# Kernel optimization log

Hardware: AMD Instinct MI355X
Metric: run time of the kernel (lower is better)

Reference implementation:

```python
import jax, jax.numpy as jnp
import numpy as np

NU, NI, DU, DI, L, FD, G, B = 100000, 50000, 128, 128, 128, 64, 3, 16384
EU, EG = 1600000, 800000


def _seg_softmax(scores, seg, n):
    # numerically stable softmax over edges grouped by destination node
    m = jax.ops.segment_max(scores, seg, num_segments=n)
    e = jnp.exp(scores - m[seg])
    s = jax.ops.segment_sum(e, seg, num_segments=n)
    return e / s[seg]


def _gat(S, W1, a_s, a_n, src, dst, n, edge_w=None):
    H1 = S @ W1                                   # [n, L]
    sc = (H1 @ a_s)[dst] + (H1 @ a_n)[src]        # [E] alpha_self_i + alpha_nb_j
    if edge_w is not None:
        sc = edge_w * sc                          # omega weighting (multi-graph)
    sc = jax.nn.leaky_relu(sc, negative_slope=0.2)
    alpha = _seg_softmax(sc, dst, n)
    return jax.ops.segment_sum(H1[src] * alpha[:, None], dst, num_segments=n)


def setup_inputs() -> dict:
    rng = np.random.default_rng(0)
    eu = rng.integers(0, NU, size=(2, EU))
    # multi-graph item edges -> coalesce (dedup, per-graph counts) as torch_geometric.coalesce reduce='add'
    e_all = rng.integers(0, NI, size=(G, 2, EG))
    src = e_all[:, 0, :].reshape(-1)
    dst = e_all[:, 1, :].reshape(-1)
    codes = dst.astype(np.int64) * NI + src
    uniq, inv = np.unique(codes, return_inverse=True)
    counts = np.zeros((uniq.size, G), np.float32)
    gid = np.repeat(np.arange(G), EG)
    np.add.at(counts, (inv, gid), 1.0)
    eb = np.stack([uniq % NI, uniq // NI]).astype(np.int64)

    key = jax.random.key(0)
    ks = jax.random.split(key, 24)
    def nrm(k, shape, s):
        return (jax.random.normal(k, shape) * s).astype(jnp.float32)
    sL = 1.0 / np.sqrt(L)
    sD = 1.0 / np.sqrt(DU)
    return {
        'user_indices': jnp.asarray(rng.integers(0, NU, B), jnp.int32),
        'item_indices': jnp.asarray(rng.integers(0, NI, B), jnp.int32),
        'S_u': nrm(ks[0], (NU, DU), 1.0),
        'S_b': nrm(ks[1], (NI, DI), 1.0),
        'edge_index_u': jnp.asarray(eu, jnp.int32),
        'edge_index_b': jnp.asarray(eb, jnp.int32),
        'graph_counts': jnp.asarray(counts),
        'W1_u': nrm(ks[2], (DU, L), sD), 'a_self_u': nrm(ks[3], (L,), sL), 'a_nb_u': nrm(ks[4], (L,), sL),
        'W1_b': nrm(ks[5], (DI, L), sD), 'a_self_b': nrm(ks[6], (L,), sL), 'a_nb_b': nrm(ks[7], (L,), sL),
        'omega': jnp.full((G,), 1.0 / G, jnp.float32),
        'W_u2': nrm(ks[8], (L, L), sL), 'W_us2_w': nrm(ks[9], (DU, L), sD), 'W_us2_b': jnp.zeros((L,), jnp.float32),
        'W_b2': nrm(ks[10], (L, L), sL), 'W_bs2_w': nrm(ks[11], (DI, L), sD), 'W_bs2_b': jnp.zeros((L,), jnp.float32),
        'W_u3': nrm(ks[12], (L, FD), sL), 'W_b3': nrm(ks[13], (L, FD), sL),
        'H_u4': nrm(ks[14], (NU, FD), 0.01), 'H_b4': nrm(ks[15], (NI, FD), 0.01),
        'bias_u': jnp.zeros((NU,), jnp.float32), 'bias_b': jnp.zeros((NI,), jnp.float32),
        'b_x': jnp.zeros((), jnp.float32),
    }


def reference(user_indices, item_indices, S_u, S_b, edge_index_u, edge_index_b, graph_counts,
              W1_u, a_self_u, a_nb_u, W1_b, a_self_b, a_nb_b, omega,
              W_u2, W_us2_w, W_us2_b, W_b2, W_bs2_w, W_bs2_b,
              W_u3, W_b3, H_u4, H_b4, bias_u, bias_b, b_x):
    Hu2 = _gat(S_u, W1_u, a_self_u, a_nb_u, edge_index_u[0], edge_index_u[1], S_u.shape[0])
    uw = graph_counts @ omega                     # coalesced omega weights per unified edge
    Hb2 = _gat(S_b, W1_b, a_self_b, a_nb_b, edge_index_b[0], edge_index_b[1], S_b.shape[0], edge_w=uw)
    Hu3 = jax.nn.elu(Hu2 @ W_u2 + S_u @ W_us2_w + W_us2_b)
    Hb3 = jax.nn.elu(Hb2 @ W_b2 + S_b @ W_bs2_w + W_bs2_b)
    U = jax.nn.elu(Hu3 @ W_u3) + H_u4
    Bm = jax.nn.elu(Hb3 @ W_b3) + H_b4
    dot = (U[user_indices] * Bm[item_indices]).sum(-1)
    raw = dot + bias_u[user_indices] + bias_b[item_indices] + b_x
    return 4.0 * jax.nn.sigmoid(raw) + 1.0        # (r_max-r_min)*sigmoid + r_min
```

## Files before the change

kernel.cpp:

```cpp
#include <hip/hip_runtime.h>
#include <hip/hip_bf16.h>

#define KD 128
#define NANF __int_as_float(0x7fc00000)

typedef __attribute__((ext_vector_type(8))) short bf16x8;
typedef __attribute__((ext_vector_type(4))) float f32x4;

__device__ __forceinline__ unsigned short f2b(float x) {
  unsigned u = __float_as_uint(x);
  return (unsigned short)((u + 0x7fffu + ((u >> 16) & 1u)) >> 16);
}
__device__ __forceinline__ int swz(int row, int kbyte) {
  return (row * 256 + kbyte) ^ ((row & 7) << 4);
}

__global__ __launch_bounds__(256) void wsplit6(
    const float* __restrict__ w0, const float* __restrict__ w1,
    const float* __restrict__ w2, const float* __restrict__ w3,
    const float* __restrict__ w4, const float* __restrict__ w5,
    unsigned short* __restrict__ oh)
{
  int m = blockIdx.x >> 6;
  int idx = (blockIdx.x & 63) * 256 + threadIdx.x;
  const float* ws;
  switch (m) { case 0: ws = w0; break; case 1: ws = w1; break; case 2: ws = w2; break;
               case 3: ws = w3; break; case 4: ws = w4; break; default: ws = w5; }
  int n = idx >> 7, k = idx & 127;
  oh[(long)m * 16384 + idx] = f2b(ws[k * 128 + n]);
}

__global__ __launch_bounds__(256) void segb_kernel(
    const int* __restrict__ dst, int E,
    int* __restrict__ sstart, int* __restrict__ send)
{
  int e = blockIdx.x * 256 + threadIdx.x;
  if (e >= E) return;
  int d = dst[e];
  if (e == 0 || dst[e - 1] != d) sstart[d] = e;
  if (e == E - 1 || dst[e + 1] != d) send[d] = e + 1;
}

__global__ __launch_bounds__(256, 3) void mfma1_dual(
    int split,
    const float* __restrict__ Aa, const unsigned short* __restrict__ Wta, int Ma,
    unsigned short* __restrict__ Ca,
    const float* __restrict__ a_sa, const float* __restrict__ a_na,
    float* __restrict__ as_oa, float* __restrict__ an_oa, const unsigned char* __restrict__ fla,
    const float* __restrict__ Ab, const unsigned short* __restrict__ Wtb, int Mb,
    unsigned short* __restrict__ Cb,
    const float* __restrict__ a_sb, const float* __restrict__ a_nb,
    float* __restrict__ as_ob, float* __restrict__ an_ob, const unsigned char* __restrict__ flb)
{
  const bool sB = (int)blockIdx.x >= split;
  const float* A = sB ? Ab : Aa;
  const unsigned short* Wt = sB ? Wtb : Wta;
  const int M = sB ? Mb : Ma;
  unsigned short* C = sB ? Cb : Ca;
  const float* a_s = sB ? a_sb : a_sa;  const float* a_n = sB ? a_nb : a_na;
  float* as_o = sB ? as_ob : as_oa;     float* an_o = sB ? an_ob : an_oa;
  const unsigned char* fl = sB ? flb : fla;
  const int bid = sB ? ((int)blockIdx.x - split) : (int)blockIdx.x;

  __shared__ unsigned short sW[16384];
  __shared__ unsigned short sA[8192];
  __shared__ float pp[4][64][2];

  const int t = threadIdx.x;
  const int w = t >> 6, l = t & 63;
  const int lr = l & 15, lk = l >> 4;
  const int row0 = bid * 64;
  char* sWc = reinterpret_cast<char*>(sW);
  char* sAc = reinterpret_cast<char*>(sA);

  #pragma unroll
  for (int q = 0; q < 8; ++q) {
    int p = t + 256 * q;
    int n = p >> 4, c16 = p & 15;
    bf16x8 v = *reinterpret_cast<const bf16x8*>(Wt + n * 128 + c16 * 8);
    *reinterpret_cast<bf16x8*>(sWc + swz(n, c16 * 16)) = v;
  }
  #pragma unroll
  for (int q = 0; q < 4; ++q) {
    int p = t + 256 * q;
    int r = p >> 4, c16 = p & 15;
    int gr = row0 + r;
    bf16x8 hv;
    if (gr < M) {
      const float4* ap = reinterpret_cast<const float4*>(A + (long)gr * KD + c16 * 8);
      float4 v0 = ap[0], v1 = ap[1];
      hv[0]=(short)f2b(v0.x); hv[1]=(short)f2b(v0.y); hv[2]=(short)f2b(v0.z); hv[3]=(short)f2b(v0.w);
      hv[4]=(short)f2b(v1.x); hv[5]=(short)f2b(v1.y); hv[6]=(short)f2b(v1.z); hv[7]=(short)f2b(v1.w);
    } else {
      #pragma unroll
      for (int j = 0; j < 8; ++j) hv[j] = 0;
    }
    *reinterpret_cast<bf16x8*>(sAc + swz(r, c16 * 16)) = hv;
  }
  __syncthreads();

  f32x4 acc[4][2];
  #pragma unroll
  for (int i = 0; i < 4; ++i)
    #pragma unroll
    for (int tt = 0; tt < 2; ++tt) acc[i][tt] = (f32x4){0.f, 0.f, 0.f, 0.f};

  #pragma unroll
  for (int kc = 0; kc < 4; ++kc) {
    const int kb = (kc * 32 + lk * 8) * 2;
    bf16x8 af[4];
    #pragma unroll
    for (int i = 0; i < 4; ++i)
      af[i] = *reinterpret_cast<const bf16x8*>(sAc + swz(i * 16 + lr, kb));
    #pragma unroll
    for (int tt = 0; tt < 2; ++tt) {
      int n = (w * 2 + tt) * 16 + lr;
      bf16x8 bfr = *reinterpret_cast<const bf16x8*>(sWc + swz(n, kb));
      #pragma unroll
      for (int i = 0; i < 4; ++i)
        acc[i][tt] = __builtin_amdgcn_mfma_f32_16x16x32_bf16(af[i], bfr, acc[i][tt], 0, 0, 0);
    }
  }

  float asv[2], anv[2];
  #pragma unroll
  for (int tt = 0; tt < 2; ++tt) {
    int col = (w * 2 + tt) * 16 + lr;
    asv[tt] = a_s[col]; anv[tt] = a_n[col];
  }
  #pragma unroll
  for (int i = 0; i < 4; ++i) {
    #pragma unroll
    for (int r = 0; r < 4; ++r) {
      float ds = acc[i][0][r] * asv[0] + acc[i][1][r] * asv[1];
      float dn = acc[i][0][r] * anv[0] + acc[i][1][r] * anv[1];
      #pragma unroll
      for (int o = 1; o < 16; o <<= 1) { ds += __shfl_xor(ds, o, 64); dn += __shfl_xor(dn, o, 64); }
      if (lr == 0) {
        int row = i * 16 + lk * 4 + r;
        pp[w][row][0] = ds; pp[w][row][1] = dn;
      }
    }
  }
  #pragma unroll
  for (int i = 0; i < 4; ++i) {
    #pragma unroll
    for (int r = 0; r < 4; ++r) {
      int gr = row0 + i * 16 + lk * 4 + r;
      if (gr >= M) continue;
      #pragma unroll
      for (int tt = 0; tt < 2; ++tt) {
        int col = (w * 2 + tt) * 16 + lr;
        C[(long)gr * 128 + col] = f2b(acc[i][tt][r]);
      }
    }
  }
  __syncthreads();
  if (t < 64) {
    int gr = row0 + t;
    if (gr < M) {
      float ds = pp[0][t][0] + pp[1][t][0] + pp[2][t][0] + pp[3][t][0];
      float dn = pp[0][t][1] + pp[1][t][1] + pp[2][t][1] + pp[3][t][1];
      as_o[gr] = fl[gr] ? ds : NANF;
      an_o[gr] = dn;
    }
  }
}

__global__ __launch_bounds__(256, 3) void mfma2_dual(
    int split,
    const float* __restrict__ A1a, const unsigned short* __restrict__ W1ta,
    const float* __restrict__ A2a, const unsigned short* __restrict__ W2ta,
    const float* __restrict__ biasa, const int* __restrict__ aidxa,
    const int* __restrict__ map1a, int Ma, float* __restrict__ Ca,
    const float* __restrict__ A1b, const unsigned short* __restrict__ W1tb,
    const float* __restrict__ A2b, const unsigned short* __restrict__ W2tb,
    const float* __restrict__ biasb, const int* __restrict__ aidxb,
    const int* __restrict__ map1b, int Mb, float* __restrict__ Cb)
{
  const bool sB = (int)blockIdx.x >= split;
  const float* A1 = sB ? A1b : A1a;  const unsigned short* W1t = sB ? W1tb : W1ta;
  const float* A2 = sB ? A2b : A2a;  const unsigned short* W2t = sB ? W2tb : W2ta;
  const float* bias = sB ? biasb : biasa;
  const int* aidx = sB ? aidxb : aidxa;  const int* map1 = sB ? map1b : map1a;
  const int M = sB ? Mb : Ma;  float* C = sB ? Cb : Ca;
  const int bid = sB ? ((int)blockIdx.x - split) : (int)blockIdx.x;

  __shared__ unsigned short sW[16384];
  __shared__ unsigned short sA[8192];

  const int t = threadIdx.x;
  const int w = t >> 6, l = t & 63;
  const int lr = l & 15, lk = l >> 4;
  const int row0 = bid * 64;
  char* sWc = reinterpret_cast<char*>(sW);
  char* sAc = reinterpret_cast<char*>(sA);

  f32x4 acc[4][2];
  #pragma unroll
  for (int i = 0; i < 4; ++i)
    #pragma unroll
    for (int tt = 0; tt < 2; ++tt) acc[i][tt] = (f32x4){0.f, 0.f, 0.f, 0.f};

  #pragma unroll
  for (int pass = 0; pass < 2; ++pass) {
    const float* Am = pass ? A2 : A1;
    const unsigned short* Wt = pass ? W2t : W1t;
    if (pass) __syncthreads();
    #pragma unroll
    for (int q = 0; q < 8; ++q) {
      int p = t + 256 * q;
      int n = p >> 4, c16 = p & 15;
      bf16x8 v = *reinterpret_cast<const bf16x8*>(Wt + n * 128 + c16 * 8);
      *reinterpret_cast<bf16x8*>(sWc + swz(n, c16 * 16)) = v;
    }
    #pragma unroll
    for (int q = 0; q < 4; ++q) {
      int p = t + 256 * q;
      int r = p >> 4, c16 = p & 15;
      int gr = row0 + r;
      bf16x8 hv;
      if (gr < M) {
        long grow = (long)aidx[gr];
        if (pass == 0) grow = map1[grow];
        const float4* ap = reinterpret_cast<const float4*>(Am + grow * KD + c16 * 8);
        float4 v0 = ap[0], v1 = ap[1];
        hv[0]=(short)f2b(v0.x); hv[1]=(short)f2b(v0.y); hv[2]=(short)f2b(v0.z); hv[3]=(short)f2b(v0.w);
        hv[4]=(short)f2b(v1.x); hv[5]=(short)f2b(v1.y); hv[6]=(short)f2b(v1.z); hv[7]=(short)f2b(v1.w);
      } else {
        #pragma unroll
        for (int j = 0; j < 8; ++j) hv[j] = 0;
      }
      *reinterpret_cast<bf16x8*>(sAc + swz(r, c16 * 16)) = hv;
    }
    __syncthreads();
    #pragma unroll
    for (int kc = 0; kc < 4; ++kc) {
      const int kb = (kc * 32 + lk * 8) * 2;
      bf16x8 af[4];
      #pragma unroll
      for (int i = 0; i < 4; ++i)
        af[i] = *reinterpret_cast<const bf16x8*>(sAc + swz(i * 16 + lr, kb));
      #pragma unroll
      for (int tt = 0; tt < 2; ++tt) {
        int n = (w * 2 + tt) * 16 + lr;
        bf16x8 bfr = *reinterpret_cast<const bf16x8*>(sWc + swz(n, kb));
        #pragma unroll
        for (int i = 0; i < 4; ++i)
          acc[i][tt] = __builtin_amdgcn_mfma_f32_16x16x32_bf16(af[i], bfr, acc[i][tt], 0, 0, 0);
      }
    }
  }
  float bv[2];
  #pragma unroll
  for (int tt = 0; tt < 2; ++tt) bv[tt] = bias[(w * 2 + tt) * 16 + lr];
  #pragma unroll
  for (int i = 0; i < 4; ++i) {
    #pragma unroll
    for (int r = 0; r < 4; ++r) {
      int gr = row0 + i * 16 + lk * 4 + r;
      if (gr >= M) continue;
      #pragma unroll
      for (int tt = 0; tt < 2; ++tt) {
        int col = (w * 2 + tt) * 16 + lr;
        float v = acc[i][tt][r] + bv[tt];
        v = (v > 0.f) ? v : (__expf(v) - 1.f);
        C[(long)gr * 128 + col] = v;
      }
    }
  }
}

template<int BM, int NC>
__global__ __launch_bounds__(256, 3) void gemm3_dual(
    int split,
    const float* __restrict__ A1a, const float* __restrict__ W1a,
    const float* __restrict__ Resa, const int* __restrict__ ridxa, int Ma,
    float* __restrict__ Ca,
    const float* __restrict__ A1b, const float* __restrict__ W1b,
    const float* __restrict__ Resb, const int* __restrict__ ridxb, int Mb,
    float* __restrict__ Cb)
{
  const bool sB = (int)blockIdx.x >= split;
  const float* A1 = sB ? A1b : A1a;  const float* W1 = sB ? W1b : W1a;
  const float* Res = sB ? Resb : Resa;
  const int* ridx = sB ? ridxb : ridxa;
  const int M = sB ? Mb : Ma;  float* C = sB ? Cb : Ca;
  const int bid = sB ? ((int)blockIdx.x - split) : (int)blockIdx.x;

  constexpr int RT = BM / 16;
  constexpr int CW = NC / 16;
  constexpr int KB = 64;
  constexpr int CPP = KD / KB;
  constexpr int F4PR = KB / 4;
  constexpr int NAF4 = BM * KB / 4 / 256;
  constexpr int NWF4 = KB * NC / 4 / 256;
  __shared__ float sA[BM][KB + 4];
  __shared__ float sW[KB][NC];
  const int t  = threadIdx.x;
  const int ty = t >> 4, tx = t & 15;
  const int row0 = bid * BM;

  float acc[RT][CW];
  #pragma unroll
  for (int i = 0; i < RT; ++i)
    #pragma unroll
    for (int j = 0; j < CW; ++j) acc[i][j] = 0.f;

  for (int cc = 0; cc < CPP; ++cc) {
    const int kc = cc;
    if (cc) __syncthreads();
    {
      const float4* Wp = reinterpret_cast<const float4*>(W1) + (long)kc * (KB * NC / 4);
      #pragma unroll
      for (int q = 0; q < NWF4; ++q)
        reinterpret_cast<float4*>(&sW[0][0])[t + 256 * q] = Wp[t + 256 * q];
    }
    #pragma unroll
    for (int q = 0; q < NAF4; ++q) {
      int p  = t + 256 * q;
      int r  = p / F4PR, c4 = p % F4PR;
      float4 v = make_float4(0.f, 0.f, 0.f, 0.f);
      int gr = row0 + r;
      if (gr < M) {
        v = reinterpret_cast<const float4*>(A1 + (long)gr * KD)[kc * F4PR + c4];
      }
      *reinterpret_cast<float4*>(&sA[r][c4 * 4]) = v;
    }
    __syncthreads();
    #pragma unroll 4
    for (int k4 = 0; k4 < KB; k4 += 4) {
      float4 a4[RT];
      #pragma unroll
      for (int i = 0; i < RT; ++i)
        a4[i] = *reinterpret_cast<const float4*>(&sA[ty + 16 * i][k4]);
      #pragma unroll
      for (int kk = 0; kk < 4; ++kk) {
        float wv[CW];
        #pragma unroll
        for (int h = 0; h < CW / 4; ++h) {
          float4 w4 = *reinterpret_cast<const float4*>(&sW[k4 + kk][tx * 4 + 64 * h]);
          wv[h*4+0] = w4.x; wv[h*4+1] = w4.y; wv[h*4+2] = w4.z; wv[h*4+3] = w4.w;
        }
        #pragma unroll
        for (int i = 0; i < RT; ++i) {
          float a = (kk == 0) ? a4[i].x : (kk == 1) ? a4[i].y : (kk == 2) ? a4[i].z : a4[i].w;
          #pragma unroll
          for (int j = 0; j < CW; ++j)
            acc[i][j] = fmaf(a, wv[j], acc[i][j]);
        }
      }
    }
  }
  #pragma unroll
  for (int i = 0; i < RT; ++i) {
    int gr = row0 + ty + 16 * i;
    if (gr >= M) continue;
    long rrow = (long)ridx[gr];
    #pragma unroll
    for (int h = 0; h < CW / 4; ++h) {
      int c = tx * 4 + 64 * h;
      float4 v = make_float4(acc[i][h*4+0], acc[i][h*4+1], acc[i][h*4+2], acc[i][h*4+3]);
      v.x = (v.x > 0.f) ? v.x : (__expf(v.x) - 1.f);
      v.y = (v.y > 0.f) ? v.y : (__expf(v.y) - 1.f);
      v.z = (v.z > 0.f) ? v.z : (__expf(v.z) - 1.f);
      v.w = (v.w > 0.f) ? v.w : (__expf(v.w) - 1.f);
      float4 rv = *reinterpret_cast<const float4*>(Res + rrow * NC + c);
      v.x += rv.x; v.y += rv.y; v.z += rv.z; v.w += rv.w;
      *reinterpret_cast<float4*>(C + (long)gr * NC + c) = v;
    }
  }
}

__global__ void flags_kernel(const int* __restrict__ ui, const int* __restrict__ ii, int B,
                             unsigned char* __restrict__ nfu, unsigned char* __restrict__ nfb,
                             unsigned* __restrict__ mku, unsigned* __restrict__ mkb)
{
  int i = blockIdx.x * blockDim.x + threadIdx.x;
  if (i < B) {
    int u = ui[i], v = ii[i];
    nfu[u] = 1; nfb[v] = 1;
    atomicOr(&mku[u >> 5], 1u << (u & 31));
    atomicOr(&mkb[v >> 5], 1u << (v & 31));
  }
}

__global__ __launch_bounds__(256) void edge_prep_dual(
    int split,
    const int* __restrict__ srcA, const int* __restrict__ dstA,
    const float* __restrict__ asA, const float* __restrict__ anA,
    const unsigned* __restrict__ mkA, const int* __restrict__ ssA,
    int* __restrict__ degA, int4* __restrict__ cmpA, int* __restrict__ bcA, int EA,
    const int* __restrict__ srcB, const int* __restrict__ dstB,
    const float* __restrict__ asB, const float* __restrict__ anB,
    const unsigned* __restrict__ mkB, const int* __restrict__ ssB,
    const float* __restrict__ gc, const float* __restrict__ omega,
    int* __restrict__ degB, int4* __restrict__ cmpB, int* __restrict__ bcB, int EB_)
{
  const bool sB = (int)blockIdx.x >= split;
  const int* src = sB ? srcB : srcA;  const int* dst = sB ? dstB : dstA;
  const float* as_ = sB ? asB : asA;  const float* an_ = sB ? anB : anA;
  const unsigned* mk = sB ? mkB : mkA;
  const int* ss = sB ? ssB : ssA;
  int* deg = sB ? degB : degA;  int4* cmp = sB ? cmpB : cmpA;
  int* blkcnt = sB ? bcB : bcA;
  const int E = sB ? EB_ : EA;
  const float* gcp = sB ? gc : nullptr;
  const int bid = sB ? ((int)blockIdx.x - split) : (int)blockIdx.x;

  __shared__ int lcnt;
  if (threadIdx.x == 0) lcnt = 0;
  __syncthreads();
  const int lane = threadIdx.x & 63;
  const long base = (long)bid * 4096;
  const int e0 = (int)base + threadIdx.x * 16;

  int d[16], s[16];
  bool act[16];
  const bool full = (e0 + 15 < E);
  if (full) {
    #pragma unroll
    for (int q = 0; q < 4; ++q) {
      int4 d4 = *reinterpret_cast<const int4*>(dst + e0 + q * 4);
      int4 s4 = *reinterpret_cast<const int4*>(src + e0 + q * 4);
      d[q*4+0]=d4.x; d[q*4+1]=d4.y; d[q*4+2]=d4.z; d[q*4+3]=d4.w;
      s[q*4+0]=s4.x; s[q*4+1]=s4.y; s[q*4+2]=s4.z; s[q*4+3]=s4.w;
    }
    #pragma unroll
    for (int j = 0; j < 16; ++j) act[j] = true;
  } else {
    #pragma unroll
    for (int j = 0; j < 16; ++j) {
      act[j] = (e0 + j < E);
      d[j] = act[j] ? dst[e0 + j] : 0;
      s[j] = act[j] ? src[e0 + j] : 0;
    }
  }
  unsigned mw[16];
  #pragma unroll
  for (int j = 0; j < 16; ++j) mw[j] = mk[d[j] >> 5];
  #pragma unroll
  for (int j = 0; j < 16; ++j) act[j] = act[j] && ((mw[j] >> (d[j] & 31)) & 1u);

  float uw[16];
  if (gcp) {
    float o0 = omega[0], o1 = omega[1], o2 = omega[2];
    if (full) {
      float g[48];
      const float4* gp = reinterpret_cast<const float4*>(gcp + (long)e0 * 3);
      #pragma unroll
      for (int q = 0; q < 12; ++q) *reinterpret_cast<float4*>(&g[q*4]) = gp[q];
      #pragma unroll
      for (int j = 0; j < 16; ++j) uw[j] = g[j*3+0]*o0 + g[j*3+1]*o1 + g[j*3+2]*o2;
    } else {
      #pragma unroll
      for (int j = 0; j < 16; ++j) {
        uw[j] = 0.f;
        if (act[j]) {
          long e = e0 + j;
          uw[j] = gcp[e*3+0]*o0 + gcp[e*3+1]*o1 + gcp[e*3+2]*o2;
        }
      }
    }
  }
  float vas[16], van[16];
  #pragma unroll
  for (int j = 0; j < 16; ++j) vas[j] = act[j] ? as_[d[j]] : 0.f;
  #pragma unroll
  for (int j = 0; j < 16; ++j) van[j] = act[j] ? an_[s[j]] : 0.f;
  int ssv[16];
  if (ss) {
    #pragma unroll
    for (int j = 0; j < 16; ++j) ssv[j] = act[j] ? ss[d[j]] : 0;
  }
  float sc[16];
  #pragma unroll
  for (int j = 0; j < 16; ++j) {
    float v = vas[j] + van[j];
    if (gcp) v *= uw[j];
    v = (v >= 0.f) ? v : 0.2f * v;
    sc[j] = __expf(v);
  }
  int tot = 0;
  #pragma unroll
  for (int j = 0; j < 16; ++j) tot += __popcll(__ballot(act[j]));
  int wb = 0;
  if (lane == 0) wb = atomicAdd(&lcnt, tot);
  wb = __shfl(wb, 0, 64);
  #pragma unroll
  for (int j = 0; j < 16; ++j) {
    unsigned long long m = __ballot(act[j]);
    if (act[j]) {
      int pref = __popcll(m & ((1ull << lane) - 1ull));
      int rel = ss ? (e0 + j - ssv[j]) : atomicAdd(&deg[d[j]], 1);
      cmp[base + wb + pref] = make_int4(s[j], d[j], rel, __float_as_int(sc[j]));
    }
    wb += __popcll(m);
  }
  __syncthreads();
  if (threadIdx.x == 0) blkcnt[bid] = lcnt;
}

__global__ __launch_bounds__(256) void offset_dual(
    int split,
    const unsigned char* __restrict__ flA, int* __restrict__ degA,
    int* __restrict__ offsA, int* __restrict__ dlA, int* __restrict__ g2cA,
    int* __restrict__ cntA, int NA,
    const unsigned char* __restrict__ flB, int* __restrict__ degB,
    const int* __restrict__ sstartB, const int* __restrict__ sendB,
    int* __restrict__ offsB, int* __restrict__ dlB, int* __restrict__ g2cB,
    int* __restrict__ cntB, int NB)
{
  const bool sB = (int)blockIdx.x >= split;
  const unsigned char* flag = sB ? flB : flA;
  int* deg = sB ? degB : degA;
  int* offs = sB ? offsB : offsA;  int* dlist = sB ? dlB : dlA;
  int* g2c = sB ? g2cB : g2cA;     int* cnt = sB ? cntB : cntA;
  const int N = sB ? NB : NA;
  const int bid = sB ? ((int)blockIdx.x - split) : (int)blockIdx.x;
  const int lane = threadIdx.x & 63;

  int idx[4], dg[4], exc[4], prf[4], nwq[4], tq[4];
  bool av[4];
  int wn = 0, wt = 0;
  #pragma unroll
  for (int q = 0; q < 4; ++q) {
    int i = bid * 1024 + q * 256 + (int)threadIdx.x;
    idx[q] = i;
    bool a = (i < N) && flag[i];
    int dgv = 0;
    if (a) {
      if (sB) { dgv = sendB[i] - sstartB[i]; deg[i] = dgv; }
      else dgv = deg[i];
    }
    av[q] = a; dg[q] = dgv;
    unsigned long long m = __ballot(a);
    nwq[q] = __popcll(m);
    prf[q] = __popcll(m & ((1ull << lane) - 1ull));
    int inc = dgv;
    #pragma unroll
    for (int o = 1; o < 64; o <<= 1) {
      int v = __shfl_up(inc, o, 64);
      if (lane >= o) inc += v;
    }
    tq[q] = __shfl(inc, 63, 64);
    exc[q] = inc - dgv;
    wn += nwq[q]; wt += tq[q];
  }
  int baseL = 0, baseE = 0;
  if (lane == 0) {
    baseL = wn ? atomicAdd(&cnt[1], wn) : 0;
    baseE = wt ? atomicAdd(&cnt[0], wt) : 0;
  }
  baseL = __shfl(baseL, 0, 64);
  baseE = __shfl(baseE, 0, 64);
  int runN = 0, runE = 0;
  #pragma unroll
  for (int q = 0; q < 4; ++q) {
    if (av[q]) {
      int i = idx[q];
      int l = baseL + runN + prf[q];
      g2c[i] = l;
      dlist[l] = i;
      if (dg[q] > 0) offs[i] = baseE + runE + exc[q];
    }
    runN += nwq[q]; runE += tq[q];
  }
}

__global__ __launch_bounds__(256) void place_dual(
    int split,
    const int4* __restrict__ cmpA, const int* __restrict__ bcA,
    const int* __restrict__ offsA, int2* __restrict__ elA,
    const int4* __restrict__ cmpB, const int* __restrict__ bcB,
    const int* __restrict__ offsB, int2* __restrict__ elB)
{
  const bool sB = (int)blockIdx.x >= split;
  const int4* cmp = sB ? cmpB : cmpA;
  const int* blkcnt = sB ? bcB : bcA;
  const int* offs = sB ? offsB : offsA;
  int2* eline = sB ? elB : elA;
  const int bid = sB ? ((int)blockIdx.x - split) : (int)blockIdx.x;

  int nb = blkcnt[bid];
  const long base = (long)bid * 4096;
  for (int k = threadIdx.x; k < nb; k += 256) {
    int4 c = cmp[base + k];
    int pos = offs[c.y] + c.z;
    eline[pos] = make_int2(c.x, c.w);
  }
}

__global__ __launch_bounds__(256) void aggr_dual(
    int split,
    const int* __restrict__ dlA, const int* __restrict__ cntA,
    const int* __restrict__ offsA, const int* __restrict__ degA,
    const int2* __restrict__ elA, const unsigned short* __restrict__ H1A, float* __restrict__ HoA,
    const int* __restrict__ dlB, const int* __restrict__ cntB,
    const int* __restrict__ offsB, const int* __restrict__ degB,
    const int2* __restrict__ elB, const unsigned short* __restrict__ H1B, float* __restrict__ HoB)
{
  const bool sB = (int)blockIdx.x >= split;
  const int* dlist = sB ? dlB : dlA;  const int* cnt = sB ? cntB : cntA;
  const int* offs = sB ? offsB : offsA;  const int* deg = sB ? degB : degA;
  const int2* eline = sB ? elB : elA;
  const unsigned short* H1 = sB ? H1B : H1A;  float* Houtc = sB ? HoB : HoA;
  const int bid = sB ? ((int)blockIdx.x - split) : (int)blockIdx.x;

  int wid  = bid * 4 + (int)(threadIdx.x >> 6);
  int lane = threadIdx.x & 63;
  if (wid >= cnt[1]) return;
  int d = dlist[wid];
  int n = deg[d];
  float2* op = reinterpret_cast<float2*>(Houtc + (long)wid * KD) + lane;
  if (n == 0) { *op = make_float2(0.f, 0.f); return; }
  int st = offs[d];
  float ssum = 0.f;
  for (int i = lane; i < n; i += 64) ssum += __int_as_float(eline[st + i].y);
  #pragma unroll
  for (int o = 32; o; o >>= 1) ssum += __shfl_xor(ssum, o, 64);
  float inv = 1.f / ssum;
  float ax = 0.f, ay = 0.f;
  int i = 0;
  for (; i + 4 <= n; i += 4) {
    int2 e0 = eline[st + i], e1 = eline[st + i + 1], e2 = eline[st + i + 2], e3 = eline[st + i + 3];
    float a0 = __int_as_float(e0.y);
    float a1 = __int_as_float(e1.y);
    float a2 = __int_as_float(e2.y);
    float a3 = __int_as_float(e3.y);
    unsigned u0 = *reinterpret_cast<const unsigned*>(H1 + (long)e0.x * KD + lane * 2);
    unsigned u1 = *reinterpret_cast<const unsigned*>(H1 + (long)e1.x * KD + lane * 2);
    unsigned u2 = *reinterpret_cast<const unsigned*>(H1 + (long)e2.x * KD + lane * 2);
    unsigned u3 = *reinterpret_cast<const unsigned*>(H1 + (long)e3.x * KD + lane * 2);
    ax = fmaf(__uint_as_float(u0 << 16), a0, ax); ay = fmaf(__uint_as_float(u0 & 0xffff0000u), a0, ay);
    ax = fmaf(__uint_as_float(u1 << 16), a1, ax); ay = fmaf(__uint_as_float(u1 & 0xffff0000u), a1, ay);
    ax = fmaf(__uint_as_float(u2 << 16), a2, ax); ay = fmaf(__uint_as_float(u2 & 0xffff0000u), a2, ay);
    ax = fmaf(__uint_as_float(u3 << 16), a3, ax); ay = fmaf(__uint_as_float(u3 & 0xffff0000u), a3, ay);
  }
  for (; i < n; ++i) {
    int2 e0 = eline[st + i];
    float a0 = __int_as_float(e0.y);
    unsigned u0 = *reinterpret_cast<const unsigned*>(H1 + (long)e0.x * KD + lane * 2);
    ax = fmaf(__uint_as_float(u0 << 16), a0, ax); ay = fmaf(__uint_as_float(u0 & 0xffff0000u), a0, ay);
  }
  *op = make_float2(ax * inv, ay * inv);
}

__global__ __launch_bounds__(256) void final_kernel(
    const float* __restrict__ Ug, const float* __restrict__ Bg,
    const int* __restrict__ ui, const int* __restrict__ ii,
    const float* __restrict__ bias_u, const float* __restrict__ bias_b,
    const float* __restrict__ bx, float* __restrict__ out, int B)
{
  int wid  = (int)((blockIdx.x * 256 + threadIdx.x) >> 6);
  int lane = threadIdx.x & 63;
  if (wid >= B) return;
  float v = Ug[(long)wid * 64 + lane] * Bg[(long)wid * 64 + lane];
  #pragma unroll
  for (int o = 32; o > 0; o >>= 1) v += __shfl_xor(v, o, 64);
  if (lane == 0) {
    float raw = v + bias_u[ui[wid]] + bias_b[ii[wid]] + bx[0];
    out[wid] = 4.f / (1.f + __expf(-raw)) + 1.f;
  }
}

extern "C" void kernel_launch(void* const* d_in, const int* in_sizes, int n_in,
                              void* d_out, int out_size, void* d_ws, size_t ws_size,
                              hipStream_t stream)
{
  const int*   ui    = (const int*)  d_in[0];
  const int*   ii    = (const int*)  d_in[1];
  const float* S_u   = (const float*)d_in[2];
  const float* S_b   = (const float*)d_in[3];
  const int*   eu    = (const int*)  d_in[4];
  const int*   eb    = (const int*)  d_in[5];
  const float* gc    = (const float*)d_in[6];
  const float* W1_u  = (const float*)d_in[7];
  const float* a_s_u = (const float*)d_in[8];
  const float* a_n_u = (const float*)d_in[9];
  const float* W1_b  = (const float*)d_in[10];
  const float* a_s_b = (const float*)d_in[11];
  const float* a_n_b = (const float*)d_in[12];
  const float* omega = (const float*)d_in[13];
  const float* W_u2  = (const float*)d_in[14];
  const float* W_us2w= (const float*)d_in[15];
  const float* W_us2b= (const float*)d_in[16];
  const float* W_b2  = (const float*)d_in[17];
  const float* W_bs2w= (const float*)d_in[18];
  const float* W_bs2b= (const float*)d_in[19];
  const float* W_u3  = (const float*)d_in[20];
  const float* W_b3  = (const float*)d_in[21];
  const float* H_u4  = (const float*)d_in[22];
  const float* H_b4  = (const float*)d_in[23];
  const float* bias_u= (const float*)d_in[24];
  const float* bias_b= (const float*)d_in[25];
  const float* b_x   = (const float*)d_in[26];
  float* out = (float*)d_out;

  const int B  = in_sizes[0];
  const int NU = in_sizes[2] / KD;
  const int NI = in_sizes[3] / KD;
  const int EU = in_sizes[4] / 2;
  const int EB = in_sizes[5] / 2;
  const int GPU_ = (EU + 4095) / 4096;
  const int GPB_ = (EB + 4095) / 4096;
  const int G1U = (NU + 63) / 64, G1I = (NI + 63) / 64;
  const int GO4U = (NU + 1023) / 1024, GO4I = (NI + 1023) / 1024;
  const int GAG = (B + 3) / 4;
  const int GB  = (B + 63) / 64;

  char* w = (char*)d_ws;
  auto alloc = [&](size_t bytes) -> void* {
    void* r = (void*)w;
    w += (bytes + 255) & ~(size_t)255;
    return r;
  };
  int* deg_u = (int*)alloc((size_t)NU * 4);
  int* deg_b = (int*)alloc((size_t)NI * 4);
  unsigned char* nfu = (unsigned char*)alloc((size_t)NU);
  unsigned char* nfb = (unsigned char*)alloc((size_t)NI);
  unsigned* mku = (unsigned*)alloc((size_t)((NU + 31) / 32) * 4);
  unsigned* mkb = (unsigned*)alloc((size_t)((NI + 31) / 32) * 4);
  int* sst_b = (int*)alloc((size_t)NI * 4);
  int* snd_b = (int*)alloc((size_t)NI * 4);
  int* cnt   = (int*)alloc(16 * 4);
  size_t zbytes = (size_t)(w - (char*)d_ws);
  unsigned short* wt = (unsigned short*)alloc((size_t)6 * 16384 * 2);
  int*   offs_u = (int*)  alloc((size_t)NU * 4);
  int*   offs_b = (int*)  alloc((size_t)NI * 4);
  int*   g2c_u  = (int*)  alloc((size_t)NU * 4);
  int*   g2c_b  = (int*)  alloc((size_t)NI * 4);
  int*   dl_u   = (int*)  alloc((size_t)B * 4);
  int*   dl_b   = (int*)  alloc((size_t)B * 4);
  int*   bc_u   = (int*)  alloc((size_t)GPU_ * 4);
  int*   bc_b   = (int*)  alloc((size_t)GPB_ * 4);
  int4*  cmp_u  = (int4*) alloc((size_t)GPU_ * 4096 * 16);
  int4*  cmp_b  = (int4*) alloc((size_t)GPB_ * 4096 * 16);
  int2*  el_u   = (int2*) alloc((size_t)EU * 8);
  int2*  el_b   = (int2*) alloc((size_t)EB * 8);
  unsigned short* H1u = (unsigned short*)alloc((size_t)NU * KD * 2);
  unsigned short* H1b = (unsigned short*)alloc((size_t)NI * KD * 2);
  float* Hu2c = (float*)alloc((size_t)B * KD * 4);
  float* Hb2c = (float*)alloc((size_t)B * KD * 4);
  float* asu  = (float*)alloc((size_t)NU * 4);
  float* anu  = (float*)alloc((size_t)NU * 4);
  float* asb  = (float*)alloc((size_t)NI * 4);
  float* anb  = (float*)alloc((size_t)NI * 4);
  float* Hu3g = (float*)alloc((size_t)B * KD * 4);
  float* Hb3g = (float*)alloc((size_t)B * KD * 4);
  float* Ug   = (float*)alloc((size_t)B * 64 * 4);
  float* Bg   = (float*)alloc((size_t)B * 64 * 4);
  (void)ws_size; (void)n_in; (void)out_size;

  hipMemsetAsync(d_ws, 0, zbytes, stream);

  wsplit6<<<384, 256, 0, stream>>>(W1_u, W1_b, W_u2, W_us2w, W_b2, W_bs2w, wt);
  flags_kernel<<<(B + 255) / 256, 256, 0, stream>>>(ui, ii, B, nfu, nfb, mku, mkb);
  segb_kernel<<<(EB + 255) / 256, 256, 0, stream>>>(eb + EB, EB, sst_b, snd_b);

  mfma1_dual<<<G1U + G1I, 256, 0, stream>>>(
      G1U,
      S_u, wt + 0 * 16384, NU, H1u, a_s_u, a_n_u, asu, anu, nfu,
      S_b, wt + 1 * 16384, NI, H1b, a_s_b, a_n_b, asb, anb, nfb);

  edge_prep_dual<<<GPU_ + GPB_, 256, 0, stream>>>(
      GPU_,
      eu, eu + EU, asu, anu, mku, nullptr, deg_u, cmp_u, bc_u, EU,
      eb, eb + EB, asb, anb, mkb, sst_b, gc, omega, deg_b, cmp_b, bc_b, EB);

  offset_dual<<<GO4U + GO4I, 256, 0, stream>>>(
      GO4U,
      nfu, deg_u, offs_u, dl_u, g2c_u, cnt + 0, NU,
      nfb, deg_b, sst_b, snd_b, offs_b, dl_b, g2c_b, cnt + 2, NI);

  place_dual<<<GPU_ + GPB_, 256, 0, stream>>>(
      GPU_,
      cmp_u, bc_u, offs_u, el_u,
      cmp_b, bc_b, offs_b, el_b);

  aggr_dual<<<GAG * 2, 256, 0, stream>>>(
      GAG,
      dl_u, cnt + 0, offs_u, deg_u, el_u, H1u, Hu2c,
      dl_b, cnt + 2, offs_b, deg_b, el_b, H1b, Hb2c);

  mfma2_dual<<<GB * 2, 256, 0, stream>>>(
      GB,
      Hu2c, wt + 2 * 16384, S_u, wt + 3 * 16384, W_us2b, ui, g2c_u, B, Hu3g,
      Hb2c, wt + 4 * 16384, S_b, wt + 5 * 16384, W_bs2b, ii, g2c_b, B, Hb3g);

  gemm3_dual<64,64><<<GB * 2, 256, 0, stream>>>(
      GB,
      Hu3g, W_u3, H_u4, ui, B, Ug,
      Hb3g, W_b3, H_b4, ii, B, Bg);

  final_kernel<<<(B + 3) / 4, 256, 0, stream>>>(Ug, Bg, ui, ii, bias_u, bias_b, b_x, out, B);
}
```

Before: 200.2 us.

## Score item-graph edges per needed destination segment instead of scanning all edges

The item-graph path no longer runs the generic edge_prep/place pipeline over every coalesced item edge. A new kernel assigns one wavefront to each destination item that is actually queried. It reads that node's contiguous, dst-sorted edge segment, computes the omega-weighted leaky-relu exp score, and writes it straight into the CSR edge list. This skips reading src/dst/graph_counts for edges whose destination is never used, and drops the compaction buffer and its write/read round trip. The user graph keeps the original path, now split into separate single-graph kernels. The cost is one extra launch, plus wave-per-node work that can be unbalanced when degrees vary.

```diff
diff --git a/kernel.cpp b/kernel.cpp
--- a/kernel.cpp
+++ b/kernel.cpp
@@ -374,44 +374,27 @@
 
 __global__ void flags_kernel(const int* __restrict__ ui, const int* __restrict__ ii, int B,
                              unsigned char* __restrict__ nfu, unsigned char* __restrict__ nfb,
-                             unsigned* __restrict__ mku, unsigned* __restrict__ mkb)
+                             unsigned* __restrict__ mku)
 {
   int i = blockIdx.x * blockDim.x + threadIdx.x;
   if (i < B) {
     int u = ui[i], v = ii[i];
     nfu[u] = 1; nfb[v] = 1;
     atomicOr(&mku[u >> 5], 1u << (u & 31));
-    atomicOr(&mkb[v >> 5], 1u << (v & 31));
-  }
-}
-
-__global__ __launch_bounds__(256) void edge_prep_dual(
-    int split,
-    const int* __restrict__ srcA, const int* __restrict__ dstA,
-    const float* __restrict__ asA, const float* __restrict__ anA,
-    const unsigned* __restrict__ mkA, const int* __restrict__ ssA,
-    int* __restrict__ degA, int4* __restrict__ cmpA, int* __restrict__ bcA, int EA,
-    const int* __restrict__ srcB, const int* __restrict__ dstB,
-    const float* __restrict__ asB, const float* __restrict__ anB,
-    const unsigned* __restrict__ mkB, const int* __restrict__ ssB,
-    const float* __restrict__ gc, const float* __restrict__ omega,
-    int* __restrict__ degB, int4* __restrict__ cmpB, int* __restrict__ bcB, int EB_)
-{
-  const bool sB = (int)blockIdx.x >= split;
-  const int* src = sB ? srcB : srcA;  const int* dst = sB ? dstB : dstA;
-  const float* as_ = sB ? asB : asA;  const float* an_ = sB ? anB : anA;
-  const unsigned* mk = sB ? mkB : mkA;
-  const int* ss = sB ? ssB : ssA;
-  int* deg = sB ? degB : degA;  int4* cmp = sB ? cmpB : cmpA;
-  int* blkcnt = sB ? bcB : bcA;
-  const int E = sB ? EB_ : EA;
-  const float* gcp = sB ? gc : nullptr;
-  const int bid = sB ? ((int)blockIdx.x - split) : (int)blockIdx.x;
-
+  }
+}
+
+__global__ __launch_bounds__(256) void edge_prep_u(
+    const int* __restrict__ src, const int* __restrict__ dst,
+    const float* __restrict__ as_, const float* __restrict__ an_,
+    const unsigned* __restrict__ mk,
+    int* __restrict__ deg, int4* __restrict__ cmp, int* __restrict__ blkcnt, int E)
+{
   __shared__ int lcnt;
   if (threadIdx.x == 0) lcnt = 0;
   __syncthreads();
   const int lane = threadIdx.x & 63;
+  const int bid = (int)blockIdx.x;
   const long base = (long)bid * 4096;
   const int e0 = (int)base + threadIdx.x * 16;
 
@@ -442,42 +425,15 @@
   #pragma unroll
   for (int j = 0; j < 16; ++j) act[j] = act[j] && ((mw[j] >> (d[j] & 31)) & 1u);
 
-  float uw[16];
-  if (gcp) {
-    float o0 = omega[0], o1 = omega[1], o2 = omega[2];
-    if (full) {
-      float g[48];
-      const float4* gp = reinterpret_cast<const float4*>(gcp + (long)e0 * 3);
-      #pragma unroll
-      for (int q = 0; q < 12; ++q) *reinterpret_cast<float4*>(&g[q*4]) = gp[q];
-      #pragma unroll
-      for (int j = 0; j < 16; ++j) uw[j] = g[j*3+0]*o0 + g[j*3+1]*o1 + g[j*3+2]*o2;
-    } else {
-      #pragma unroll
-      for (int j = 0; j < 16; ++j) {
-        uw[j] = 0.f;
-        if (act[j]) {
-          long e = e0 + j;
-          uw[j] = gcp[e*3+0]*o0 + gcp[e*3+1]*o1 + gcp[e*3+2]*o2;
-        }
-      }
-    }
-  }
   float vas[16], van[16];
   #pragma unroll
   for (int j = 0; j < 16; ++j) vas[j] = act[j] ? as_[d[j]] : 0.f;
   #pragma unroll
   for (int j = 0; j < 16; ++j) van[j] = act[j] ? an_[s[j]] : 0.f;
-  int ssv[16];
-  if (ss) {
-    #pragma unroll
-    for (int j = 0; j < 16; ++j) ssv[j] = act[j] ? ss[d[j]] : 0;
-  }
   float sc[16];
   #pragma unroll
   for (int j = 0; j < 16; ++j) {
     float v = vas[j] + van[j];
-    if (gcp) v *= uw[j];
     v = (v >= 0.f) ? v : 0.2f * v;
     sc[j] = __expf(v);
   }
@@ -492,7 +448,7 @@
     unsigned long long m = __ballot(act[j]);
     if (act[j]) {
       int pref = __popcll(m & ((1ull << lane) - 1ull));
-      int rel = ss ? (e0 + j - ssv[j]) : atomicAdd(&deg[d[j]], 1);
+      int rel = atomicAdd(&deg[d[j]], 1);
       cmp[base + wb + pref] = make_int4(s[j], d[j], rel, __float_as_int(sc[j]));
     }
     wb += __popcll(m);
@@ -568,26 +524,43 @@
   }
 }
 
-__global__ __launch_bounds__(256) void place_dual(
-    int split,
-    const int4* __restrict__ cmpA, const int* __restrict__ bcA,
-    const int* __restrict__ offsA, int2* __restrict__ elA,
-    const int4* __restrict__ cmpB, const int* __restrict__ bcB,
-    const int* __restrict__ offsB, int2* __restrict__ elB)
-{
-  const bool sB = (int)blockIdx.x >= split;
-  const int4* cmp = sB ? cmpB : cmpA;
-  const int* blkcnt = sB ? bcB : bcA;
-  const int* offs = sB ? offsB : offsA;
-  int2* eline = sB ? elB : elA;
-  const int bid = sB ? ((int)blockIdx.x - split) : (int)blockIdx.x;
-
-  int nb = blkcnt[bid];
-  const long base = (long)bid * 4096;
+__global__ __launch_bounds__(256) void place_u(
+    const int4* __restrict__ cmp, const int* __restrict__ blkcnt,
+    const int* __restrict__ offs, int2* __restrict__ eline)
+{
+  int nb = blkcnt[blockIdx.x];
+  const long base = (long)blockIdx.x * 4096;
   for (int k = threadIdx.x; k < nb; k += 256) {
     int4 c = cmp[base + k];
     int pos = offs[c.y] + c.z;
     eline[pos] = make_int2(c.x, c.w);
+  }
+}
+
+__global__ __launch_bounds__(256) void edge_scoreb(
+    const int* __restrict__ src, const float* __restrict__ as_, const float* __restrict__ an_,
+    const float* __restrict__ gc, const float* __restrict__ omega,
+    const int* __restrict__ dl, const int* __restrict__ cnt, const int* __restrict__ offs,
+    const int* __restrict__ sstart, const int* __restrict__ send,
+    int2* __restrict__ eline)
+{
+  int wid  = (int)blockIdx.x * 4 + (int)(threadIdx.x >> 6);
+  int lane = threadIdx.x & 63;
+  if (wid >= cnt[1]) return;
+  int d = dl[wid];
+  int st = sstart[d], en = send[d];
+  int n = en - st;
+  if (n <= 0) return;
+  int ob = offs[d];
+  float asd = as_[d];
+  float o0 = omega[0], o1 = omega[1], o2 = omega[2];
+  for (int i = lane; i < n; i += 64) {
+    long e = st + i;
+    int s = src[e];
+    float uw = gc[e*3+0]*o0 + gc[e*3+1]*o1 + gc[e*3+2]*o2;
+    float v = (asd + an_[s]) * uw;
+    v = (v >= 0.f) ? v : 0.2f * v;
+    eline[ob + i] = make_int2(s, __float_as_int(__expf(v)));
   }
 }
 
@@ -703,7 +676,6 @@
   const int EU = in_sizes[4] / 2;
   const int EB = in_sizes[5] / 2;
   const int GPU_ = (EU + 4095) / 4096;
-  const int GPB_ = (EB + 4095) / 4096;
   const int G1U = (NU + 63) / 64, G1I = (NI + 63) / 64;
   const int GO4U = (NU + 1023) / 1024, GO4I = (NI + 1023) / 1024;
   const int GAG = (B + 3) / 4;
@@ -720,7 +692,6 @@
   unsigned char* nfu = (unsigned char*)alloc((size_t)NU);
   unsigned char* nfb = (unsigned char*)alloc((size_t)NI);
   unsigned* mku = (unsigned*)alloc((size_t)((NU + 31) / 32) * 4);
-  unsigned* mkb = (unsigned*)alloc((size_t)((NI + 31) / 32) * 4);
   int* sst_b = (int*)alloc((size_t)NI * 4);
   int* snd_b = (int*)alloc((size_t)NI * 4);
   int* cnt   = (int*)alloc(16 * 4);
@@ -733,9 +704,7 @@
   int*   dl_u   = (int*)  alloc((size_t)B * 4);
   int*   dl_b   = (int*)  alloc((size_t)B * 4);
   int*   bc_u   = (int*)  alloc((size_t)GPU_ * 4);
-  int*   bc_b   = (int*)  alloc((size_t)GPB_ * 4);
   int4*  cmp_u  = (int4*) alloc((size_t)GPU_ * 4096 * 16);
-  int4*  cmp_b  = (int4*) alloc((size_t)GPB_ * 4096 * 16);
   int2*  el_u   = (int2*) alloc((size_t)EU * 8);
   int2*  el_b   = (int2*) alloc((size_t)EB * 8);
   unsigned short* H1u = (unsigned short*)alloc((size_t)NU * KD * 2);
@@ -755,7 +724,7 @@
   hipMemsetAsync(d_ws, 0, zbytes, stream);
 
   wsplit6<<<384, 256, 0, stream>>>(W1_u, W1_b, W_u2, W_us2w, W_b2, W_bs2w, wt);
-  flags_kernel<<<(B + 255) / 256, 256, 0, stream>>>(ui, ii, B, nfu, nfb, mku, mkb);
+  flags_kernel<<<(B + 255) / 256, 256, 0, stream>>>(ui, ii, B, nfu, nfb, mku);
   segb_kernel<<<(EB + 255) / 256, 256, 0, stream>>>(eb + EB, EB, sst_b, snd_b);
 
   mfma1_dual<<<G1U + G1I, 256, 0, stream>>>(
@@ -763,20 +732,18 @@
       S_u, wt + 0 * 16384, NU, H1u, a_s_u, a_n_u, asu, anu, nfu,
       S_b, wt + 1 * 16384, NI, H1b, a_s_b, a_n_b, asb, anb, nfb);
 
-  edge_prep_dual<<<GPU_ + GPB_, 256, 0, stream>>>(
-      GPU_,
-      eu, eu + EU, asu, anu, mku, nullptr, deg_u, cmp_u, bc_u, EU,
-      eb, eb + EB, asb, anb, mkb, sst_b, gc, omega, deg_b, cmp_b, bc_b, EB);
+  edge_prep_u<<<GPU_, 256, 0, stream>>>(
+      eu, eu + EU, asu, anu, mku, deg_u, cmp_u, bc_u, EU);
 
   offset_dual<<<GO4U + GO4I, 256, 0, stream>>>(
       GO4U,
       nfu, deg_u, offs_u, dl_u, g2c_u, cnt + 0, NU,
       nfb, deg_b, sst_b, snd_b, offs_b, dl_b, g2c_b, cnt + 2, NI);
 
-  place_dual<<<GPU_ + GPB_, 256, 0, stream>>>(
-      GPU_,
-      cmp_u, bc_u, offs_u, el_u,
-      cmp_b, bc_b, offs_b, el_b);
+  place_u<<<GPU_, 256, 0, stream>>>(cmp_u, bc_u, offs_u, el_u);
+
+  edge_scoreb<<<GAG, 256, 0, stream>>>(
+      eb, asb, anb, gc, omega, dl_b, cnt + 2, offs_b, sst_b, snd_b, el_b);
 
   aggr_dual<<<GAG * 2, 256, 0, stream>>>(
       GAG,
```

Measured after the change: 191.1 us. -4.6%, faster.
